# Performance work log

Hardware: AMD Instinct MI355X
Metric: run time of the kernel (lower is better)

Reference implementation:

```python
import jax, jax.numpy as jnp
import numpy as np

B, N, C = 16, 4096, 512
H = 8                      # num_heads
HEIGHT = WIDTH = 64        # input_resolution, HEIGHT*WIDTH == N
D = C // H                 # head_dim = 64
SCALE = D ** (-0.25)       # head_dim ** -0.25 (applied to both axial logits)


def setup_inputs() -> dict:
    key = jax.random.key(0)
    k0, k1, k2 = jax.random.split(key, 3)
    return {
        "x": jax.random.normal(k0, (B, N, C), jnp.float32),
        "W_qkv": jax.random.normal(k1, (C, 3 * C), jnp.float32) / np.sqrt(C).astype(np.float32),
        "b_qkv": jnp.zeros((3 * C,), jnp.float32),
        "W_proj": jax.random.normal(k2, (C, C), jnp.float32) / np.sqrt(C).astype(np.float32),
        "b_proj": jnp.zeros((C,), jnp.float32),
    }


def reference(x, W_qkv, b_qkv, W_proj, b_proj):
    Bx, Nx, Cx = x.shape
    # qkv projection -> [3, B, H, height, width, D]
    qkv = (x @ W_qkv + b_qkv).reshape(Bx, Nx, 3, H, D)
    qkv = jnp.transpose(qkv, (2, 0, 3, 1, 4)).reshape(3, Bx, H, HEIGHT, WIDTH, D)
    q, k, v = qkv[0], qkv[1], qkv[2]

    # row attention (channel_merge='concat'): contract over (width, channel)
    a = jnp.einsum('bhiwc,bhjwc->bhij', q, k) * SCALE          # [B,H,height,height]
    a = jax.nn.softmax(a, axis=-1)
    # column attention: contract over (height, channel)
    bm = jnp.einsum('bhtic,bhtjc->bhij', q, k) * SCALE         # [B,H,width,width]
    bm = jax.nn.softmax(bm, axis=-1)

    # coupled combination: (v_perm @ b^T) then a @ (...)
    # tmp[b,h,c,t,u] = sum_w v[b,h,t,w,c] * bm[b,h,u,w]
    tmp = jnp.einsum('bhtwc,bhuw->bhctu', v, bm)               # [B,H,D,height,width]
    out = jnp.einsum('bhij,bhcjw->bhciw', a, tmp)              # [B,H,D,height,width]

    out = out.reshape(Bx, Cx, Nx).transpose(0, 2, 1)           # [B,N,C]
    return out @ W_proj + b_proj
```

## Files before the change

### kernel.cpp

```cpp
#include <hip/hip_runtime.h>
#include <math.h>

#define SCALE_F 0.35355339059327373f

typedef unsigned short u16;
typedef unsigned int   u32;
typedef _Float16 f16;
typedef _Float16 f16x8 __attribute__((ext_vector_type(8)));
typedef float    f32x4 __attribute__((ext_vector_type(4)));

__device__ __forceinline__ u16 f2h(float f) { f16 h = (f16)f; return *(u16*)&h; }
__device__ __forceinline__ float h2f(u16 b) { f16 h = *(f16*)&b; return (float)h; }

__device__ __forceinline__ void glds16(const u16* g, char* l) {
    __builtin_amdgcn_global_load_lds((const __attribute__((address_space(1))) void*)g,
                                     (__attribute__((address_space(3))) void*)l, 16, 0, 0);
}
__device__ __forceinline__ f32x4 mfma16(f16x8 a, f16x8 b, f32x4 c) {
    return __builtin_amdgcn_mfma_f32_16x16x32_f16(a, b, c, 0, 0, 0);
}

__global__ __launch_bounds__(256) void to_f16(
    const float* __restrict__ X, u16* __restrict__ out)
{
    size_t i = ((size_t)blockIdx.x * 256 + threadIdx.x) * 8;
    float4 a = *(const float4*)(X + i);
    float4 b = *(const float4*)(X + i + 4);
    ushort4 r0, r1;
    r0.x = f2h(a.x); r0.y = f2h(a.y); r0.z = f2h(a.z); r0.w = f2h(a.w);
    r1.x = f2h(b.x); r1.y = f2h(b.y); r1.z = f2h(b.z); r1.w = f2h(b.w);
    *(ushort4*)(out + i)     = r0;
    *(ushort4*)(out + i + 4) = r1;
}

__global__ __launch_bounds__(256) void transpose_f16(
    const float* __restrict__ in, u16* __restrict__ out, int R, int C)
{
    __shared__ __align__(16) u16 T[64 * 80];
    const int c0 = blockIdx.x * 64, r0 = blockIdx.y * 64, z = blockIdx.z;
    const int t = threadIdx.x;
    const int rl = t >> 4, c4 = (t & 15) * 4;
    const float* base = in + (size_t)z * R * C;

    #pragma unroll
    for (int rr = 0; rr < 4; ++rr) {
        int r = rr * 16 + rl;
        float4 v = *(const float4*)(base + (size_t)(r0 + r) * C + c0 + c4);
        T[(c4 + 0) * 80 + r] = f2h(v.x);
        T[(c4 + 1) * 80 + r] = f2h(v.y);
        T[(c4 + 2) * 80 + r] = f2h(v.z);
        T[(c4 + 3) * 80 + r] = f2h(v.w);
    }
    __syncthreads();
    #pragma unroll
    for (int rep = 0; rep < 2; ++rep) {
        int idx = rep * 256 + t;
        int cl = idx >> 3, r8 = (idx & 7) * 8;
        *(float4*)(out + ((size_t)z * C + c0 + cl) * R + r0 + r8) =
            *(const float4*)&T[cl * 80 + r8];
    }
}

__global__ __launch_bounds__(256) void transpose16(
    const u16* __restrict__ in, u16* __restrict__ out)
{
    __shared__ __align__(16) u16 T[64 * 80];
    const int c0 = blockIdx.x * 64, r0 = blockIdx.y * 64, z = blockIdx.z;
    const int t = threadIdx.x;
    const int rl = t >> 3;
    const int c8 = (t & 7) * 8;
    const u16* base = in + (size_t)z * 512 * 4096;

    #pragma unroll
    for (int rr = 0; rr < 2; ++rr) {
        int r = rr * 32 + rl;
        const u16* p = base + (size_t)(r0 + r) * 4096 + c0 + c8;
        ushort4 v0 = *(const ushort4*)(p);
        ushort4 v1 = *(const ushort4*)(p + 4);
        T[(c8 + 0) * 80 + r] = v0.x;
        T[(c8 + 1) * 80 + r] = v0.y;
        T[(c8 + 2) * 80 + r] = v0.z;
        T[(c8 + 3) * 80 + r] = v0.w;
        T[(c8 + 4) * 80 + r] = v1.x;
        T[(c8 + 5) * 80 + r] = v1.y;
        T[(c8 + 6) * 80 + r] = v1.z;
        T[(c8 + 7) * 80 + r] = v1.w;
    }
    __syncthreads();
    #pragma unroll
    for (int rep = 0; rep < 2; ++rep) {
        int idx = rep * 256 + t;
        int cl = idx >> 3, r8 = (idx & 7) * 8;
        *(float4*)(out + ((size_t)z * 4096 + c0 + cl) * 512 + r0 + r8) =
            *(const float4*)&T[cl * 80 + r8];
    }
}

__global__ __launch_bounds__(256) void qkv_mfma(
    const u16* __restrict__ Xh, const u16* __restrict__ WT,
    const float* __restrict__ bias,
    u16* __restrict__ Q, u16* __restrict__ Kk, u16* __restrict__ Vt)
{
    __shared__ __align__(16) char smem[33280];
    char* As = smem;
    char* Bs = smem + 16384;

    const int nt = blockIdx.x, mt = blockIdx.y;
    const int t = threadIdx.x;
    const int wave = t >> 6, lane = t & 63;
    const int wm = wave & 1, wn = wave >> 1;
    const int quad = lane >> 4, l16 = lane & 15;
    const int m0 = mt * 128;

    size_t xoff[4], woff[4];
    int lb[4];
    #pragma unroll
    for (int r = 0; r < 4; ++r) {
        const int row = wm * 64 + lane;
        const int oct = r * 2 + wn;
        xoff[r] = (size_t)(m0 + row) * 512 + oct * 8;
        woff[r] = (size_t)(nt * 128 + row) * 512 + oct * 8;
        lb[r]   = (r * 256 + wave * 64) * 16;
    }

    f32x4 acc[4][4];
    #pragma unroll
    for (int i = 0; i < 4; ++i)
        #pragma unroll
        for (int j = 0; j < 4; ++j) acc[i][j] = (f32x4){0.f, 0.f, 0.f, 0.f};

    for (int k0 = 0; k0 < 512; k0 += 64) {
        __syncthreads();
        #pragma unroll
        for (int r = 0; r < 4; ++r) {
            glds16(Xh + xoff[r] + k0, As + lb[r]);
            glds16(WT + woff[r] + k0, Bs + lb[r]);
        }
        __syncthreads();

        #pragma unroll
        for (int ss = 0; ss < 2; ++ss) {
            f16x8 af[4], bf[4];
            #pragma unroll
            for (int i = 0; i < 4; ++i)
                af[i] = *(const f16x8*)(As + (((ss * 4 + quad) * 128) + wm * 64 + i * 16 + l16) * 16);
            #pragma unroll
            for (int j = 0; j < 4; ++j)
                bf[j] = *(const f16x8*)(Bs + (((ss * 4 + quad) * 128) + wn * 64 + j * 16 + l16) * 16);
            #pragma unroll
            for (int i = 0; i < 4; ++i)
                #pragma unroll
                for (int j = 0; j < 4; ++j)
                    acc[i][j] = mfma16(af[i], bf[j], acc[i][j]);
        }
    }

    const int b   = m0 >> 12;
    const int nn0 = m0 & 4095;
    float bv[4];
    #pragma unroll
    for (int j = 0; j < 4; ++j) bv[j] = bias[nt * 128 + wn * 64 + j * 16 + l16];

    if (nt < 8) {
        u16* dst = (nt < 4) ? Q : Kk;
        const int colbase = (nt & 3) * 128;
        #pragma unroll
        for (int i = 0; i < 4; ++i) {
            const int rowb = wm * 64 + i * 16 + quad * 4;
            #pragma unroll
            for (int j = 0; j < 4; ++j) {
                const int col = colbase + wn * 64 + j * 16 + l16;
                const int h = col >> 6, d = col & 63;
                u16* p = dst + ((size_t)((b * 8 + h) * 4096 + nn0 + rowb)) * 64 + d;
                #pragma unroll
                for (int r = 0; r < 4; ++r)
                    p[(size_t)r * 64] = f2h(acc[i][j][r] + bv[j]);
            }
        }
    } else {
        float* Tr = (float*)smem;
        #pragma unroll
        for (int g = 0; g < 2; ++g) {
            __syncthreads();
            if (wn == g) {
                #pragma unroll
                for (int i = 0; i < 4; ++i)
                    #pragma unroll
                    for (int j = 0; j < 4; ++j)
                        #pragma unroll
                        for (int r = 0; r < 4; ++r)
                            Tr[(wm * 64 + i * 16 + quad * 4 + r) * 65 + j * 16 + l16] =
                                acc[i][j][r] + bv[j];
            }
            __syncthreads();
            const int h = (nt & 3) * 2 + g;
            u16* dstv = Vt + ((size_t)(b * 8 + h) * 64) * 4096 + nn0;
            #pragma unroll
            for (int rep = 0; rep < 32; ++rep) {
                int idx = rep * 256 + t;
                int d = idx >> 7, rr = idx & 127;
                dstv[(size_t)d * 4096 + rr] = f2h(Tr[rr * 65 + d]);
            }
        }
    }
}

__global__ __launch_bounds__(256) void attn_logits(
    const u16* __restrict__ Q, const u16* __restrict__ Kk,
    float* __restrict__ Aout, float* __restrict__ Bmout)
{
    __shared__ float sm[64 * 68];
    __shared__ float red[128];

    const int bh   = blockIdx.x;
    const int mode = blockIdx.y;
    const int t    = threadIdx.x;
    const int wave = t >> 6, lane = t & 63;
    const int wr = wave & 1, wc = wave >> 1;
    const int quad = lane >> 4, l16 = lane & 15;

    const u16* Qb = Q  + (size_t)bh * 262144;
    const u16* Kb = Kk + (size_t)bh * 262144;

    const int rA0 = wr * 32 + l16, rA1 = rA0 + 16;
    const int rB0 = wc * 32 + l16, rB1 = rB0 + 16;

    f32x4 acc[2][2];
    #pragma unroll
    for (int i = 0; i < 2; ++i)
        #pragma unroll
        for (int j = 0; j < 2; ++j) acc[i][j] = (f32x4){0.f, 0.f, 0.f, 0.f};

    if (mode == 0) {
        const u16* pA0 = Qb + (size_t)rA0 * 4096;
        const u16* pA1 = Qb + (size_t)rA1 * 4096;
        const u16* pB0 = Kb + (size_t)rB0 * 4096;
        const u16* pB1 = Kb + (size_t)rB1 * 4096;
        #pragma unroll 4
        for (int k0 = 0; k0 < 4096; k0 += 32) {
            const int kk = k0 + quad * 8;
            f16x8 a0 = *(const f16x8*)(pA0 + kk);
            f16x8 a1 = *(const f16x8*)(pA1 + kk);
            f16x8 b0 = *(const f16x8*)(pB0 + kk);
            f16x8 b1 = *(const f16x8*)(pB1 + kk);
            acc[0][0] = mfma16(a0, b0, acc[0][0]);
            acc[0][1] = mfma16(a0, b1, acc[0][1]);
            acc[1][0] = mfma16(a1, b0, acc[1][0]);
            acc[1][1] = mfma16(a1, b1, acc[1][1]);
        }
    } else {
        #pragma unroll 4
        for (int k0 = 0; k0 < 4096; k0 += 32) {
            const int kk = k0 + quad * 8;
            const size_t base = (size_t)(kk >> 6) * 4096 + (kk & 63);
            f16x8 a0 = *(const f16x8*)(Qb + base + rA0 * 64);
            f16x8 a1 = *(const f16x8*)(Qb + base + rA1 * 64);
            f16x8 b0 = *(const f16x8*)(Kb + base + rB0 * 64);
            f16x8 b1 = *(const f16x8*)(Kb + base + rB1 * 64);
            acc[0][0] = mfma16(a0, b0, acc[0][0]);
            acc[0][1] = mfma16(a0, b1, acc[0][1]);
            acc[1][0] = mfma16(a1, b0, acc[1][0]);
            acc[1][1] = mfma16(a1, b1, acc[1][1]);
        }
    }

    #pragma unroll
    for (int i = 0; i < 2; ++i)
        #pragma unroll
        for (int j = 0; j < 2; ++j)
            #pragma unroll
            for (int r = 0; r < 4; ++r)
                sm[(wr * 32 + i * 16 + quad * 4 + r) * 68 + wc * 32 + j * 16 + l16] =
                    acc[i][j][r] * SCALE_F;
    __syncthreads();
    if (t < 64) {
        float m = -1e30f;
        for (int j = 0; j < 64; ++j) m = fmaxf(m, sm[t * 68 + j]);
        float ssum = 0.f;
        for (int j = 0; j < 64; ++j) ssum += __expf(sm[t * 68 + j] - m);
        red[t] = m;
        red[64 + t] = 1.0f / ssum;
    }
    __syncthreads();
    float* Out = ((mode == 0) ? Aout : Bmout) + (size_t)bh * 4096;
    #pragma unroll
    for (int rep = 0; rep < 16; ++rep) {
        int idx = rep * 256 + t;
        int i = idx >> 6, j = idx & 63;
        Out[idx] = __expf(sm[i * 68 + j] - red[i]) * red[64 + i];
    }
}

__global__ __launch_bounds__(256) void coupling(
    const u16* __restrict__ Vt, const float* __restrict__ Aatt,
    const float* __restrict__ Bm, u16* __restrict__ Yh)
{
    __shared__ __align__(16) u16 Ah[64 * 72];
    __shared__ __align__(16) u16 Bh[64 * 72];
    __shared__ __align__(16) u16 Tt[2][64 * 72];

    const int bh = blockIdx.x, cg = blockIdx.y;
    const int t = threadIdx.x;
    const int wave = t >> 6, lane = t & 63;
    const int wr = wave & 1, wc = wave >> 1;
    const int quad = lane >> 4, l16 = lane & 15;

    const float* Ab = Aatt + (size_t)bh * 4096;
    const float* Bb = Bm   + (size_t)bh * 4096;
    const u16*  Vb  = Vt   + (size_t)bh * 262144;
    u16* Yb = Yh + (size_t)bh * 262144;

    {
        const int row = t >> 2;
        const int colb = (t & 3) * 16;
        #pragma unroll
        for (int q = 0; q < 4; ++q) {
            float4 va = *(const float4*)(Ab + (size_t)row * 64 + colb + q * 4);
            Ah[row * 72 + colb + q * 4 + 0] = f2h(va.x);
            Ah[row * 72 + colb + q * 4 + 1] = f2h(va.y);
            Ah[row * 72 + colb + q * 4 + 2] = f2h(va.z);
            Ah[row * 72 + colb + q * 4 + 3] = f2h(va.w);
            float4 vb = *(const float4*)(Bb + (size_t)row * 64 + colb + q * 4);
            Bh[row * 72 + colb + q * 4 + 0] = f2h(vb.x);
            Bh[row * 72 + colb + q * 4 + 1] = f2h(vb.y);
            Bh[row * 72 + colb + q * 4 + 2] = f2h(vb.z);
            Bh[row * 72 + colb + q * 4 + 3] = f2h(vb.w);
        }
    }
    __syncthreads();

    for (int ci = 0; ci < 16; ++ci) {
        const int c = cg * 16 + ci;
        u16* tb = &Tt[ci & 1][0];

        f32x4 acc1[2][2];
        #pragma unroll
        for (int i = 0; i < 2; ++i)
            #pragma unroll
            for (int j = 0; j < 2; ++j) acc1[i][j] = (f32x4){0.f, 0.f, 0.f, 0.f};
        #pragma unroll
        for (int s = 0; s < 2; ++s) {
            f16x8 a1[2], b1[2];
            #pragma unroll
            for (int i = 0; i < 2; ++i)
                a1[i] = *(const f16x8*)&Bh[(wr * 32 + i * 16 + l16) * 72 + s * 32 + quad * 8];
            #pragma unroll
            for (int j = 0; j < 2; ++j)
                b1[j] = *(const f16x8*)(Vb + (size_t)c * 4096 +
                                        (size_t)(wc * 32 + j * 16 + l16) * 64 + s * 32 + quad * 8);
            #pragma unroll
            for (int i = 0; i < 2; ++i)
                #pragma unroll
                for (int j = 0; j < 2; ++j)
                    acc1[i][j] = mfma16(a1[i], b1[j], acc1[i][j]);
        }
        #pragma unroll
        for (int i = 0; i < 2; ++i)
            #pragma unroll
            for (int j = 0; j < 2; ++j)
                #pragma unroll
                for (int r = 0; r < 4; ++r)
                    tb[(wr * 32 + i * 16 + quad * 4 + r) * 72 + wc * 32 + j * 16 + l16] =
                        f2h(acc1[i][j][r]);
        __syncthreads();

        f32x4 acc2[2][2];
        #pragma unroll
        for (int i = 0; i < 2; ++i)
            #pragma unroll
            for (int j = 0; j < 2; ++j) acc2[i][j] = (f32x4){0.f, 0.f, 0.f, 0.f};
        #pragma unroll
        for (int s = 0; s < 2; ++s) {
            f16x8 a2[2], b2[2];
            #pragma unroll
            for (int i = 0; i < 2; ++i)
                a2[i] = *(const f16x8*)&Ah[(wr * 32 + i * 16 + l16) * 72 + s * 32 + quad * 8];
            #pragma unroll
            for (int u = 0; u < 2; ++u)
                b2[u] = *(const f16x8*)&tb[(wc * 32 + u * 16 + l16) * 72 + s * 32 + quad * 8];
            #pragma unroll
            for (int i = 0; i < 2; ++i)
                #pragma unroll
                for (int u = 0; u < 2; ++u)
                    acc2[i][u] = mfma16(a2[i], b2[u], acc2[i][u]);
        }
        #pragma unroll
        for (int i = 0; i < 2; ++i)
            #pragma unroll
            for (int u = 0; u < 2; ++u)
                #pragma unroll
                for (int r = 0; r < 4; ++r)
                    Yb[(size_t)c * 4096 + (wr * 32 + i * 16 + quad * 4 + r) * 64 +
                       wc * 32 + u * 16 + l16] = f2h(acc2[i][u][r]);
    }
}

__global__ __launch_bounds__(256) void proj_mfma(
    const u16* __restrict__ A, const u16* __restrict__ WT,
    const float* __restrict__ bias, float* __restrict__ Out)
{
    __shared__ __align__(16) char smem[32768];
    char* As = smem;
    char* Bs = smem + 16384;

    const int nt = blockIdx.x, mt = blockIdx.y;
    const int t = threadIdx.x;
    const int wave = t >> 6, lane = t & 63;
    const int wm = wave & 1, wn = wave >> 1;
    const int quad = lane >> 4, l16 = lane & 15;
    const int m0 = mt * 128;

    size_t aoff[4], woff[4];
    int lb[4];
    #pragma unroll
    for (int r = 0; r < 4; ++r) {
        const int row = wm * 64 + lane;
        const int oct = r * 2 + wn;
        aoff[r] = (size_t)(m0 + row) * 512 + oct * 8;
        woff[r] = (size_t)(nt * 128 + row) * 512 + oct * 8;
        lb[r]   = (r * 256 + wave * 64) * 16;
    }

    f32x4 acc[4][4];
    #pragma unroll
    for (int i = 0; i < 4; ++i)
        #pragma unroll
        for (int j = 0; j < 4; ++j) acc[i][j] = (f32x4){0.f, 0.f, 0.f, 0.f};

    for (int k0 = 0; k0 < 512; k0 += 64) {
        __syncthreads();
        #pragma unroll
        for (int r = 0; r < 4; ++r) {
            glds16(A + aoff[r] + k0,  As + lb[r]);
            glds16(WT + woff[r] + k0, Bs + lb[r]);
        }
        __syncthreads();

        #pragma unroll
        for (int ss = 0; ss < 2; ++ss) {
            f16x8 af[4], bf[4];
            #pragma unroll
            for (int i = 0; i < 4; ++i)
                af[i] = *(const f16x8*)(As + (((ss * 4 + quad) * 128) + wm * 64 + i * 16 + l16) * 16);
            #pragma unroll
            for (int j = 0; j < 4; ++j)
                bf[j] = *(const f16x8*)(Bs + (((ss * 4 + quad) * 128) + wn * 64 + j * 16 + l16) * 16);
            #pragma unroll
            for (int i = 0; i < 4; ++i)
                #pragma unroll
                for (int j = 0; j < 4; ++j)
                    acc[i][j] = mfma16(af[i], bf[j], acc[i][j]);
        }
    }

    float bv[4];
    #pragma unroll
    for (int j = 0; j < 4; ++j) bv[j] = bias[nt * 128 + wn * 64 + j * 16 + l16];

    #pragma unroll
    for (int i = 0; i < 4; ++i) {
        const int rowb = m0 + wm * 64 + i * 16 + quad * 4;
        #pragma unroll
        for (int j = 0; j < 4; ++j) {
            const int col = nt * 128 + wn * 64 + j * 16 + l16;
            #pragma unroll
            for (int r = 0; r < 4; ++r)
                Out[(size_t)(rowb + r) * 512 + col] = acc[i][j][r] + bv[j];
        }
    }
}

extern "C" void kernel_launch(void* const* d_in, const int* in_sizes, int n_in,
                              void* d_out, int out_size, void* d_ws, size_t ws_size,
                              hipStream_t stream)
{
    const float* x     = (const float*)d_in[0];
    const float* Wqkv  = (const float*)d_in[1];
    const float* bqkv  = (const float*)d_in[2];
    const float* Wproj = (const float*)d_in[3];
    const float* bproj = (const float*)d_in[4];
    float* out = (float*)d_out;

    u16* Xh  = (u16*)d_ws;
    u16* Qh  = Xh + 33554432;
    u16* Kh  = Qh + 33554432;
    u16* Vth = Kh + 33554432;
    u16* WqT = Vth + 33554432;
    u16* WpT = WqT + 786432;
    float* Aa = (float*)(WpT + 262144);
    float* Bm = Aa + 524288;
    u16* Yh  = Xh;
    u16* Ytb = Kh;

    to_f16        <<<16384, 256, 0, stream>>>(x, Xh);
    transpose_f16 <<<dim3(24, 8, 1),  256, 0, stream>>>(Wqkv,  WqT, 512, 1536);
    transpose_f16 <<<dim3(8, 8, 1),   256, 0, stream>>>(Wproj, WpT, 512, 512);
    qkv_mfma      <<<dim3(12, 512),   256, 0, stream>>>(Xh, WqT, bqkv, Qh, Kh, Vth);
    attn_logits   <<<dim3(128, 2),    256, 0, stream>>>(Qh, Kh, Aa, Bm);
    coupling      <<<dim3(128, 4),    256, 0, stream>>>(Vth, Aa, Bm, Yh);
    transpose16   <<<dim3(64, 8, 16), 256, 0, stream>>>(Yh, Ytb);
    proj_mfma     <<<dim3(4, 512),    256, 0, stream>>>(Ytb, WpT, bproj, out);
}
```

Baseline: 714.7 us.

## Double-buffer GEMM LDS loads and remap blocks for XCD-local L2 reuse

Both the QKV and output-projection GEMM kernels now use a K-step of 32 with two LDS buffers. The next tile is loaded asynchronously via global_load_lds while the current one feeds the MFMAs, which cuts the two barriers per step down to one. The launch grid is flattened to 1D and block ids are remapped so that consecutive row tiles land on the same XCD, aiming for better L2 reuse of the shared activation rows. The risks are more loop iterations with smaller MFMA batches per barrier, and a reliance on round-robin dispatch of blocks across XCDs.

```diff
diff --git a/kernel.cpp b/kernel.cpp
--- a/kernel.cpp
+++ b/kernel.cpp
@@ -102,26 +102,27 @@
     u16* __restrict__ Q, u16* __restrict__ Kk, u16* __restrict__ Vt)
 {
     __shared__ __align__(16) char smem[33280];
-    char* As = smem;
-    char* Bs = smem + 16384;
-
-    const int nt = blockIdx.x, mt = blockIdx.y;
+
+    const int id  = blockIdx.x;
+    const int xcd = id & 7;
+    const int jj  = id >> 3;
+    const int mt  = xcd * 64 + jj / 12;
+    const int nt  = jj % 12;
+
     const int t = threadIdx.x;
     const int wave = t >> 6, lane = t & 63;
     const int wm = wave & 1, wn = wave >> 1;
     const int quad = lane >> 4, l16 = lane & 15;
     const int m0 = mt * 128;
 
-    size_t xoff[4], woff[4];
-    int lb[4];
-    #pragma unroll
-    for (int r = 0; r < 4; ++r) {
-        const int row = wm * 64 + lane;
-        const int oct = r * 2 + wn;
-        xoff[r] = (size_t)(m0 + row) * 512 + oct * 8;
-        woff[r] = (size_t)(nt * 128 + row) * 512 + oct * 8;
-        lb[r]   = (r * 256 + wave * 64) * 16;
-    }
+    const int c0 = wave * 128 + lane;
+    const int c1 = c0 + 64;
+    const size_t xoff0 = (size_t)(m0 + (c0 & 127)) * 512 + (c0 >> 7) * 8;
+    const size_t xoff1 = (size_t)(m0 + (c1 & 127)) * 512 + (c1 >> 7) * 8;
+    const size_t woff0 = (size_t)(nt * 128 + (c0 & 127)) * 512 + (c0 >> 7) * 8;
+    const size_t woff1 = (size_t)(nt * 128 + (c1 & 127)) * 512 + (c1 >> 7) * 8;
+    const int lb0 = (wave * 128) * 16;
+    const int lb1 = lb0 + 64 * 16;
 
     f32x4 acc[4][4];
     #pragma unroll
@@ -129,30 +130,38 @@
         #pragma unroll
         for (int j = 0; j < 4; ++j) acc[i][j] = (f32x4){0.f, 0.f, 0.f, 0.f};
 
-    for (int k0 = 0; k0 < 512; k0 += 64) {
+    glds16(Xh + xoff0, smem + lb0);
+    glds16(Xh + xoff1, smem + lb1);
+    glds16(WT + woff0, smem + 8192 + lb0);
+    glds16(WT + woff1, smem + 8192 + lb1);
+    __syncthreads();
+
+    for (int k0 = 0; k0 < 512; k0 += 32) {
+        const int co = (k0 & 32) << 9;
+        const int cn = co ^ 16384;
+        char* Ac = smem + co;
+        char* Bc = smem + 8192 + co;
+        if (k0 < 480) {
+            glds16(Xh + xoff0 + k0 + 32, smem + cn + lb0);
+            glds16(Xh + xoff1 + k0 + 32, smem + cn + lb1);
+            glds16(WT + woff0 + k0 + 32, smem + 8192 + cn + lb0);
+            glds16(WT + woff1 + k0 + 32, smem + 8192 + cn + lb1);
+        }
+
+        f16x8 af[4], bf[4];
+        #pragma unroll
+        for (int i = 0; i < 4; ++i)
+            af[i] = *(const f16x8*)(Ac + (quad * 128 + wm * 64 + i * 16 + l16) * 16);
+        #pragma unroll
+        for (int j = 0; j < 4; ++j)
+            bf[j] = *(const f16x8*)(Bc + (quad * 128 + wn * 64 + j * 16 + l16) * 16);
+        #pragma unroll
+        for (int i = 0; i < 4; ++i)
+            #pragma unroll
+            for (int j = 0; j < 4; ++j)
+                acc[i][j] = mfma16(af[i], bf[j], acc[i][j]);
+
         __syncthreads();
-        #pragma unroll
-        for (int r = 0; r < 4; ++r) {
-            glds16(Xh + xoff[r] + k0, As + lb[r]);
-            glds16(WT + woff[r] + k0, Bs + lb[r]);
-        }
-        __syncthreads();
-
-        #pragma unroll
-        for (int ss = 0; ss < 2; ++ss) {
-            f16x8 af[4], bf[4];
-            #pragma unroll
-            for (int i = 0; i < 4; ++i)
-                af[i] = *(const f16x8*)(As + (((ss * 4 + quad) * 128) + wm * 64 + i * 16 + l16) * 16);
-            #pragma unroll
-            for (int j = 0; j < 4; ++j)
-                bf[j] = *(const f16x8*)(Bs + (((ss * 4 + quad) * 128) + wn * 64 + j * 16 + l16) * 16);
-            #pragma unroll
-            for (int i = 0; i < 4; ++i)
-                #pragma unroll
-                for (int j = 0; j < 4; ++j)
-                    acc[i][j] = mfma16(af[i], bf[j], acc[i][j]);
-        }
     }
 
     const int b   = m0 >> 12;
@@ -400,26 +409,27 @@
     const float* __restrict__ bias, float* __restrict__ Out)
 {
     __shared__ __align__(16) char smem[32768];
-    char* As = smem;
-    char* Bs = smem + 16384;
-
-    const int nt = blockIdx.x, mt = blockIdx.y;
+
+    const int id  = blockIdx.x;
+    const int xcd = id & 7;
+    const int jj  = id >> 3;
+    const int mt  = xcd * 64 + (jj >> 2);
+    const int nt  = jj & 3;
+
     const int t = threadIdx.x;
     const int wave = t >> 6, lane = t & 63;
     const int wm = wave & 1, wn = wave >> 1;
     const int quad = lane >> 4, l16 = lane & 15;
     const int m0 = mt * 128;
 
-    size_t aoff[4], woff[4];
-    int lb[4];
-    #pragma unroll
-    for (int r = 0; r < 4; ++r) {
-        const int row = wm * 64 + lane;
-        const int oct = r * 2 + wn;
-        aoff[r] = (size_t)(m0 + row) * 512 + oct * 8;
-        woff[r] = (size_t)(nt * 128 + row) * 512 + oct * 8;
-        lb[r]   = (r * 256 + wave * 64) * 16;
-    }
+    const int c0 = wave * 128 + lane;
+    const int c1 = c0 + 64;
+    const size_t aoff0 = (size_t)(m0 + (c0 & 127)) * 512 + (c0 >> 7) * 8;
+    const size_t aoff1 = (size_t)(m0 + (c1 & 127)) * 512 + (c1 >> 7) * 8;
+    const size_t woff0 = (size_t)(nt * 128 + (c0 & 127)) * 512 + (c0 >> 7) * 8;
+    const size_t woff1 = (size_t)(nt * 128 + (c1 & 127)) * 512 + (c1 >> 7) * 8;
+    const int lb0 = (wave * 128) * 16;
+    const int lb1 = lb0 + 64 * 16;
 
     f32x4 acc[4][4];
     #pragma unroll
@@ -427,30 +437,38 @@
         #pragma unroll
         for (int j = 0; j < 4; ++j) acc[i][j] = (f32x4){0.f, 0.f, 0.f, 0.f};
 
-    for (int k0 = 0; k0 < 512; k0 += 64) {
+    glds16(A  + aoff0, smem + lb0);
+    glds16(A  + aoff1, smem + lb1);
+    glds16(WT + woff0, smem + 8192 + lb0);
+    glds16(WT + woff1, smem + 8192 + lb1);
+    __syncthreads();
+
+    for (int k0 = 0; k0 < 512; k0 += 32) {
+        const int co = (k0 & 32) << 9;
+        const int cn = co ^ 16384;
+        char* Ac = smem + co;
+        char* Bc = smem + 8192 + co;
+        if (k0 < 480) {
+            glds16(A  + aoff0 + k0 + 32, smem + cn + lb0);
+            glds16(A  + aoff1 + k0 + 32, smem + cn + lb1);
+            glds16(WT + woff0 + k0 + 32, smem + 8192 + cn + lb0);
+            glds16(WT + woff1 + k0 + 32, smem + 8192 + cn + lb1);
+        }
+
+        f16x8 af[4], bf[4];
+        #pragma unroll
+        for (int i = 0; i < 4; ++i)
+            af[i] = *(const f16x8*)(Ac + (quad * 128 + wm * 64 + i * 16 + l16) * 16);
+        #pragma unroll
+        for (int j = 0; j < 4; ++j)
+            bf[j] = *(const f16x8*)(Bc + (quad * 128 + wn * 64 + j * 16 + l16) * 16);
+        #pragma unroll
+        for (int i = 0; i < 4; ++i)
+            #pragma unroll
+            for (int j = 0; j < 4; ++j)
+                acc[i][j] = mfma16(af[i], bf[j], acc[i][j]);
+
         __syncthreads();
-        #pragma unroll
-        for (int r = 0; r < 4; ++r) {
-            glds16(A + aoff[r] + k0,  As + lb[r]);
-            glds16(WT + woff[r] + k0, Bs + lb[r]);
-        }
-        __syncthreads();
-
-        #pragma unroll
-        for (int ss = 0; ss < 2; ++ss) {
-            f16x8 af[4], bf[4];
-            #pragma unroll
-            for (int i = 0; i < 4; ++i)
-                af[i] = *(const f16x8*)(As + (((ss * 4 + quad) * 128) + wm * 64 + i * 16 + l16) * 16);
-            #pragma unroll
-            for (int j = 0; j < 4; ++j)
-                bf[j] = *(const f16x8*)(Bs + (((ss * 4 + quad) * 128) + wn * 64 + j * 16 + l16) * 16);
-            #pragma unroll
-            for (int i = 0; i < 4; ++i)
-                #pragma unroll
-                for (int j = 0; j < 4; ++j)
-                    acc[i][j] = mfma16(af[i], bf[j], acc[i][j]);
-        }
     }
 
     float bv[4];
@@ -495,9 +513,9 @@
     to_f16        <<<16384, 256, 0, stream>>>(x, Xh);
     transpose_f16 <<<dim3(24, 8, 1),  256, 0, stream>>>(Wqkv,  WqT, 512, 1536);
     transpose_f16 <<<dim3(8, 8, 1),   256, 0, stream>>>(Wproj, WpT, 512, 512);
-    qkv_mfma      <<<dim3(12, 512),   256, 0, stream>>>(Xh, WqT, bqkv, Qh, Kh, Vth);
+    qkv_mfma      <<<6144,            256, 0, stream>>>(Xh, WqT, bqkv, Qh, Kh, Vth);
     attn_logits   <<<dim3(128, 2),    256, 0, stream>>>(Qh, Kh, Aa, Bm);
     coupling      <<<dim3(128, 4),    256, 0, stream>>>(Vth, Aa, Bm, Yh);
     transpose16   <<<dim3(64, 8, 16), 256, 0, stream>>>(Yh, Ytb);
-    proj_mfma     <<<dim3(4, 512),    256, 0, stream>>>(Ytb, WpT, bproj, out);
-}
+    proj_mfma     <<<2048,            256, 0, stream>>>(Ytb, WpT, bproj, out);
+}
```

Measured after the change: 678.6 us. -5.1%, faster.
